# Kernel tuning notes

Hardware: AMD Instinct MI355X
Metric: run time of the kernel (lower is better)

The kernel has to match this reference:

```python
import jax, jax.numpy as jnp
import numpy as np

EPS = 1e-12  # F.normalize clamp eps
LOGIT_SCALE = float(np.exp(np.log(100.0)))  # coattn_logit_scale.exp() == 100.0


def _l2norm(x):
    n = jnp.linalg.norm(x, axis=-1, keepdims=True)
    return x / jnp.maximum(n, EPS)


def setup_inputs() -> dict:
    key = jax.random.key(0)
    k1, k2, k3, k4 = jax.random.split(key, 4)
    B, N, C = 1, 100000, 1024
    NUM_QUERY = 10  # +1 gated query
    X = jax.random.normal(k1, (B, N, C), dtype=jnp.float32)
    Q = jax.random.normal(k2, (NUM_QUERY + 1, C), dtype=jnp.float32)
    W = jax.random.normal(k3, (C, C), dtype=jnp.float32) * (1.0 / np.sqrt(C))
    b = jax.random.normal(k4, (C,), dtype=jnp.float32) * 0.01
    return {"X": X, "Q": Q, "W": W, "b": b}


def reference(X, Q, W, b):
    # X: [1, N, C] bag features; Q: [num_query+1, C]; W,b: visual_adapter Linear
    Qn = _l2norm(Q)[None]            # [1, q+1, C]
    Xn = _l2norm(X)                  # [1, N, C]
    A_ = jnp.einsum('bqc,bnc->bqn', Qn, Xn)   # cosine similarities [1, q+1, N]
    # gated-query subtraction: last query's scores subtracted from the rest
    A_ = A_[:, :-1, :] - A_[:, -1:, :]        # [1, q, N]
    A = jax.nn.softmax(LOGIT_SCALE * A_, axis=-1)
    out = jnp.einsum('bqn,bnc->bqc', A, X)    # [1, q, C]
    pooled = jnp.mean(out, axis=1)            # 'mean' query pooling -> [1, C]
    return pooled @ W.T + b                   # visual_adapter (nn.Linear)
```

## Files before the change

### kernel.cpp

```cpp
#include <hip/hip_runtime.h>
#include <float.h>
#include <math.h>

#define C    1024
#define NQ   10
#define LGS  16
#define K1B  2048
#define K1W  (K1B * 4)
#define G4   512

template <int CTRL, int ROWM>
__device__ __forceinline__ float dpp_add(float x) {
  int mv = __builtin_amdgcn_update_dpp(0, __float_as_int(x), CTRL, ROWM, 0xf, true);
  return x + __int_as_float(mv);
}
__device__ __forceinline__ float wave_sum64(float x) {
  x = dpp_add<0xB1,  0xf>(x);
  x = dpp_add<0x4E,  0xf>(x);
  x = dpp_add<0x141, 0xf>(x);
  x = dpp_add<0x140, 0xf>(x);
  x = dpp_add<0x142, 0xa>(x);
  x = dpp_add<0x143, 0xc>(x);
  return __int_as_float(__builtin_amdgcn_readlane(__float_as_int(x), 63));
}

__global__ __launch_bounds__(256) void k0_qdiff(const float* __restrict__ Q,
                                                float* __restrict__ qd) {
  __shared__ float red[256];
  __shared__ float inorm[NQ + 1];
  int t = threadIdx.x;
  for (int k = 0; k <= NQ; ++k) {
    float s = 0.f;
    for (int c = t; c < C; c += 256) { float v = Q[k * C + c]; s = fmaf(v, v, s); }
    red[t] = s; __syncthreads();
    for (int st = 128; st > 0; st >>= 1) {
      if (t < st) red[t] += red[t + st];
      __syncthreads();
    }
    if (t == 0) inorm[k] = 1.0f / fmaxf(sqrtf(red[0]), 1e-12f);
    __syncthreads();
  }
  for (int k = 0; k < NQ; ++k)
    for (int c = t; c < C; c += 256)
      qd[k * C + c] = Q[k * C + c] * inorm[k] - Q[NQ * C + c] * inorm[NQ];
}

__global__ __launch_bounds__(256) void k1_logits(const float* __restrict__ X,
                                                 const float* __restrict__ qd,
                                                 float* __restrict__ Lg,
                                                 float* __restrict__ bmax,
                                                 int N) {
  const int t  = threadIdx.x;
  const int l  = t & 63, wv = t >> 6;
  const int w  = blockIdx.x * 4 + wv;
  const int co = l << 2;

  float4 q4[NQ][4];
#pragma unroll
  for (int k = 0; k < NQ; ++k)
#pragma unroll
    for (int j = 0; j < 4; ++j)
      q4[k][j] = *(const float4*)(qd + k * C + j * 256 + co);

  float mx[NQ];
#pragma unroll
  for (int k = 0; k < NQ; ++k) mx[k] = -FLT_MAX;

  for (int r = w; r < N; r += K1W) {
    const float* xp = X + (size_t)r * C + co;
    float4 xv[4];
#pragma unroll
    for (int j = 0; j < 4; ++j) xv[j] = *(const float4*)(xp + j * 256);

    float ss = 0.f;
    float dot[NQ];
#pragma unroll
    for (int k = 0; k < NQ; ++k) dot[k] = 0.f;
#pragma unroll
    for (int j = 0; j < 4; ++j) {
      float4 v = xv[j];
      ss = fmaf(v.x, v.x, fmaf(v.y, v.y, fmaf(v.z, v.z, fmaf(v.w, v.w, ss))));
#pragma unroll
      for (int k = 0; k < NQ; ++k) {
        float4 q = q4[k][j];
        dot[k] = fmaf(v.x, q.x, fmaf(v.y, q.y, fmaf(v.z, q.z, fmaf(v.w, q.w, dot[k]))));
      }
    }

    float ssu = wave_sum64(ss);
    float rn  = 100.0f / fmaxf(sqrtf(ssu), 1e-12f);
    float lg[NQ];
#pragma unroll
    for (int k = 0; k < NQ; ++k) {
      lg[k] = wave_sum64(dot[k]) * rn;
      mx[k] = fmaxf(mx[k], lg[k]);
    }
    if (l == 0) {
      float* lp = Lg + (size_t)r * LGS;
      *(float4*)(lp)     = make_float4(lg[0], lg[1], lg[2], lg[3]);
      *(float4*)(lp + 4) = make_float4(lg[4], lg[5], lg[6], lg[7]);
      *(float2*)(lp + 8) = make_float2(lg[8], lg[9]);
    }
  }

  __shared__ float sm[4][16];
  if (l == 0) {
#pragma unroll
    for (int k = 0; k < NQ; ++k) sm[wv][k] = mx[k];
  }
  __syncthreads();
  if (t < NQ) {
    float m = fmaxf(fmaxf(sm[0][t], sm[1][t]), fmaxf(sm[2][t], sm[3][t]));
    bmax[blockIdx.x * 16 + t] = m;
  }
}

__global__ __launch_bounds__(256) void k2_gmax(const float* __restrict__ bmax,
                                               float* __restrict__ M, int NB) {
  __shared__ float red[256];
  int k = blockIdx.x, t = threadIdx.x;
  float mm = -FLT_MAX;
  for (int i = t; i < NB; i += 256) mm = fmaxf(mm, bmax[i * 16 + k]);
  red[t] = mm; __syncthreads();
  for (int st = 128; st > 0; st >>= 1) {
    if (t < st) red[t] = fmaxf(red[t], red[t + st]);
    __syncthreads();
  }
  if (t == 0) M[k] = red[0];
}

__global__ __launch_bounds__(256) void k4_partial(const float* __restrict__ X,
                                                  const float* __restrict__ Lg,
                                                  const float* __restrict__ M,
                                                  float* __restrict__ partial,
                                                  float* __restrict__ dsum,
                                                  int N, int rpb) {
  int g = blockIdx.x, t = threadIdx.x;
  int n0 = g * rpb;
  int n1 = min(n0 + rpb, N);
  float m[NQ];
#pragma unroll
  for (int k = 0; k < NQ; ++k) m[k] = M[k];
  float a[NQ][4];
#pragma unroll
  for (int k = 0; k < NQ; ++k) { a[k][0] = 0.f; a[k][1] = 0.f; a[k][2] = 0.f; a[k][3] = 0.f; }
  float ds[NQ];
#pragma unroll
  for (int k = 0; k < NQ; ++k) ds[k] = 0.f;

#pragma unroll 2
  for (int n = n0; n < n1; ++n) {
    float4 x4 = *(const float4*)&X[(size_t)n * C + (t << 2)];
    float w[NQ];
#pragma unroll
    for (int k = 0; k < NQ; ++k) w[k] = __expf(Lg[(size_t)n * LGS + k] - m[k]);
#pragma unroll
    for (int k = 0; k < NQ; ++k) {
      ds[k] += w[k];
      a[k][0] = fmaf(w[k], x4.x, a[k][0]);
      a[k][1] = fmaf(w[k], x4.y, a[k][1]);
      a[k][2] = fmaf(w[k], x4.z, a[k][2]);
      a[k][3] = fmaf(w[k], x4.w, a[k][3]);
    }
  }
#pragma unroll
  for (int k = 0; k < NQ; ++k) {
    float4 o; o.x = a[k][0]; o.y = a[k][1]; o.z = a[k][2]; o.w = a[k][3];
    *(float4*)&partial[(((size_t)(g * NQ + k)) << 10) + (t << 2)] = o;
  }
  if (t == 0) {
#pragma unroll
    for (int k = 0; k < NQ; ++k) dsum[g * NQ + k] = ds[k];
  }
}

__global__ __launch_bounds__(256) void k5a_pooled(const float* __restrict__ partial,
                                                  const float* __restrict__ dsum,
                                                  float* __restrict__ pooled) {
  __shared__ float invD[NQ];
  __shared__ float r4[256][4];
  int t = threadIdx.x;
  if (t < NQ) {
    float s = 0.f;
    for (int g = 0; g < G4; ++g) s += dsum[g * NQ + t];
    invD[t] = 1.0f / (s * (float)NQ);
  }
  __syncthreads();
  int c0 = blockIdx.x * 4;
  float a0 = 0.f, a1 = 0.f, a2 = 0.f, a3 = 0.f;
  for (int idx = t; idx < G4 * NQ; idx += 256) {
    int k = idx % NQ;
    const float4 p = *(const float4*)&partial[(((size_t)idx) << 10) + c0];
    float s = invD[k];
    a0 = fmaf(p.x, s, a0); a1 = fmaf(p.y, s, a1);
    a2 = fmaf(p.z, s, a2); a3 = fmaf(p.w, s, a3);
  }
  r4[t][0] = a0; r4[t][1] = a1; r4[t][2] = a2; r4[t][3] = a3;
  __syncthreads();
  for (int st = 128; st > 0; st >>= 1) {
    if (t < st) {
      r4[t][0] += r4[t + st][0]; r4[t][1] += r4[t + st][1];
      r4[t][2] += r4[t + st][2]; r4[t][3] += r4[t + st][3];
    }
    __syncthreads();
  }
  if (t < 4) pooled[c0 + t] = r4[0][t];
}

__global__ __launch_bounds__(256) void k5b_out(const float* __restrict__ W,
                                               const float* __restrict__ bias,
                                               const float* __restrict__ pooled,
                                               float* __restrict__ out) {
  __shared__ float sp[C];
  int t = threadIdx.x;
  for (int i = t; i < C; i += 256) sp[i] = pooled[i];
  __syncthreads();
  int wv = t >> 6, lane = t & 63;
#pragma unroll
  for (int jj = 0; jj < 8; ++jj) {
    int j = blockIdx.x * 32 + wv * 8 + jj;
    float s = 0.f;
#pragma unroll
    for (int seg = 0; seg < 4; ++seg) {
      int cbase = seg * 256 + lane * 4;
      float4 w4 = *(const float4*)&W[(size_t)j * C + cbase];
      float4 p4 = *(const float4*)&sp[cbase];
      s += w4.x * p4.x + w4.y * p4.y + w4.z * p4.z + w4.w * p4.w;
    }
#pragma unroll
    for (int off = 32; off > 0; off >>= 1) s += __shfl_down(s, off);
    if (lane == 0) out[j] = s + bias[j];
  }
}

extern "C" void kernel_launch(void* const* d_in, const int* in_sizes, int n_in,
                              void* d_out, int out_size, void* d_ws, size_t ws_size,
                              hipStream_t stream) {
  const float* X = (const float*)d_in[0];
  const float* Q = (const float*)d_in[1];
  const float* W = (const float*)d_in[2];
  const float* b = (const float*)d_in[3];
  float* out = (float*)d_out;

  int N = in_sizes[0] / C;
  int rpb = (N + G4 - 1) / G4;

  float* ws      = (float*)d_ws;
  float* qd      = ws;
  float* M       = qd + NQ * C;
  float* bmax    = M + 16;
  float* dsum    = bmax + K1B * 16;
  float* pooled  = dsum + G4 * NQ;
  float* Lg      = pooled + C;
  float* partial = Lg + (size_t)N * LGS;

  hipLaunchKernelGGL(k0_qdiff,  dim3(1),      dim3(256), 0, stream, Q, qd);
  hipLaunchKernelGGL(k1_logits, dim3(K1B),    dim3(256), 0, stream, X, qd, Lg, bmax, N);
  hipLaunchKernelGGL(k2_gmax,   dim3(NQ),     dim3(256), 0, stream, bmax, M, K1B);
  hipLaunchKernelGGL(k4_partial,dim3(G4),     dim3(256), 0, stream, X, Lg, M, partial, dsum, N, rpb);
  hipLaunchKernelGGL(k5a_pooled,dim3(C / 4),  dim3(256), 0, stream, partial, dsum, pooled);
  hipLaunchKernelGGL(k5b_out,   dim3(C / 32), dim3(256), 0, stream, W, b, pooled, out);
}
```

Before: 747.7 us.

## Fuse logit and weighted-sum passes with online softmax per block

Merges the logit kernel, the global-max kernel and the partial-accumulation kernel into one kernel that runs online softmax. Each block handles a contiguous row range in chunks of 25 rows: it computes logits into LDS, rescales its accumulators whenever the running max changes, then accumulates exp-weighted X while the chunk is still hot in cache. The pooling kernel then merges per-block maxima and rescales the partial sums. This removes the second full HBM read of X (about 400MB) and the logits buffer round-trip. The cost is extra block-wide syncs per chunk and only 500 blocks, each with heavy register pressure.

```diff
diff --git a/kernel.cpp b/kernel.cpp
--- a/kernel.cpp
+++ b/kernel.cpp
@@ -4,10 +4,9 @@
 
 #define C    1024
 #define NQ   10
+#define G4   500
 #define LGS  16
-#define K1B  2048
-#define K1W  (K1B * 4)
-#define G4   512
+#define RSUB 25
 
 template <int CTRL, int ROWM>
 __device__ __forceinline__ float dpp_add(float x) {
@@ -45,124 +44,120 @@
       qd[k * C + c] = Q[k * C + c] * inorm[k] - Q[NQ * C + c] * inorm[NQ];
 }
 
-__global__ __launch_bounds__(256) void k1_logits(const float* __restrict__ X,
-                                                 const float* __restrict__ qd,
-                                                 float* __restrict__ Lg,
-                                                 float* __restrict__ bmax,
-                                                 int N) {
-  const int t  = threadIdx.x;
-  const int l  = t & 63, wv = t >> 6;
-  const int w  = blockIdx.x * 4 + wv;
+__global__ __launch_bounds__(256, 2) void kf_fused(const float* __restrict__ X,
+                                                   const float* __restrict__ qd,
+                                                   float* __restrict__ partial,
+                                                   float* __restrict__ dsum,
+                                                   float* __restrict__ mblk,
+                                                   int N, int rpb) {
+  __shared__ float lgbuf[2][RSUB][LGS];
+  __shared__ float wmS[4][8];
+  __shared__ float sMnew[16];
+
+  const int g = blockIdx.x, t = threadIdx.x;
+  const int l = t & 63, wv = t >> 6;
+  const int pr = wv >> 1;
+  const int qbase = (wv & 1) * 5;
   const int co = l << 2;
 
-  float4 q4[NQ][4];
-#pragma unroll
-  for (int k = 0; k < NQ; ++k)
+  const int n0 = g * rpb;
+  const int n1 = min(n0 + rpb, N);
+
+  float4 q4[5][4];
+#pragma unroll
+  for (int k = 0; k < 5; ++k)
 #pragma unroll
     for (int j = 0; j < 4; ++j)
-      q4[k][j] = *(const float4*)(qd + k * C + j * 256 + co);
-
-  float mx[NQ];
-#pragma unroll
-  for (int k = 0; k < NQ; ++k) mx[k] = -FLT_MAX;
-
-  for (int r = w; r < N; r += K1W) {
-    const float* xp = X + (size_t)r * C + co;
-    float4 xv[4];
-#pragma unroll
-    for (int j = 0; j < 4; ++j) xv[j] = *(const float4*)(xp + j * 256);
-
-    float ss = 0.f;
-    float dot[NQ];
-#pragma unroll
-    for (int k = 0; k < NQ; ++k) dot[k] = 0.f;
-#pragma unroll
-    for (int j = 0; j < 4; ++j) {
-      float4 v = xv[j];
-      ss = fmaf(v.x, v.x, fmaf(v.y, v.y, fmaf(v.z, v.z, fmaf(v.w, v.w, ss))));
-#pragma unroll
-      for (int k = 0; k < NQ; ++k) {
-        float4 q = q4[k][j];
-        dot[k] = fmaf(v.x, q.x, fmaf(v.y, q.y, fmaf(v.z, q.z, fmaf(v.w, q.w, dot[k]))));
+      q4[k][j] = *(const float4*)(qd + (qbase + k) * C + j * 256 + co);
+
+  float a[NQ][4], ds[NQ], mo[NQ];
+#pragma unroll
+  for (int k = 0; k < NQ; ++k) {
+    a[k][0] = a[k][1] = a[k][2] = a[k][3] = 0.f;
+    ds[k] = 0.f; mo[k] = -FLT_MAX;
+  }
+
+  int s = 0;
+  for (int c0 = n0; c0 < n1; c0 += RSUB) {
+    const int cnt = min(RSUB, n1 - c0);
+
+    float wmx[5];
+#pragma unroll
+    for (int k = 0; k < 5; ++k) wmx[k] = -FLT_MAX;
+
+    for (int i = pr; i < cnt; i += 2) {
+      const float* xp = X + (size_t)(c0 + i) * C + co;
+      float4 xv[4];
+#pragma unroll
+      for (int j = 0; j < 4; ++j) xv[j] = *(const float4*)(xp + j * 256);
+
+      float ss = 0.f, dot[5];
+#pragma unroll
+      for (int k = 0; k < 5; ++k) dot[k] = 0.f;
+#pragma unroll
+      for (int j = 0; j < 4; ++j) {
+        float4 v = xv[j];
+        ss = fmaf(v.x, v.x, fmaf(v.y, v.y, fmaf(v.z, v.z, fmaf(v.w, v.w, ss))));
+#pragma unroll
+        for (int k = 0; k < 5; ++k) {
+          float4 q = q4[k][j];
+          dot[k] = fmaf(v.x, q.x, fmaf(v.y, q.y, fmaf(v.z, q.z, fmaf(v.w, q.w, dot[k]))));
+        }
       }
-    }
-
-    float ssu = wave_sum64(ss);
-    float rn  = 100.0f / fmaxf(sqrtf(ssu), 1e-12f);
-    float lg[NQ];
+      float ssu = wave_sum64(ss);
+      float rn  = 100.0f / fmaxf(sqrtf(ssu), 1e-12f);
+#pragma unroll
+      for (int k = 0; k < 5; ++k) {
+        float lg = wave_sum64(dot[k]) * rn;
+        wmx[k] = fmaxf(wmx[k], lg);
+        if (l == 0) lgbuf[s][i][qbase + k] = lg;
+      }
+    }
+    if (l == 0) {
+#pragma unroll
+      for (int k = 0; k < 5; ++k) wmS[wv][k] = wmx[k];
+    }
+    __syncthreads();
+
 #pragma unroll
     for (int k = 0; k < NQ; ++k) {
-      lg[k] = wave_sum64(dot[k]) * rn;
-      mx[k] = fmaxf(mx[k], lg[k]);
-    }
-    if (l == 0) {
-      float* lp = Lg + (size_t)r * LGS;
-      *(float4*)(lp)     = make_float4(lg[0], lg[1], lg[2], lg[3]);
-      *(float4*)(lp + 4) = make_float4(lg[4], lg[5], lg[6], lg[7]);
-      *(float2*)(lp + 8) = make_float2(lg[8], lg[9]);
-    }
-  }
-
-  __shared__ float sm[4][16];
-  if (l == 0) {
-#pragma unroll
-    for (int k = 0; k < NQ; ++k) sm[wv][k] = mx[k];
-  }
-  __syncthreads();
-  if (t < NQ) {
-    float m = fmaxf(fmaxf(sm[0][t], sm[1][t]), fmaxf(sm[2][t], sm[3][t]));
-    bmax[blockIdx.x * 16 + t] = m;
-  }
-}
-
-__global__ __launch_bounds__(256) void k2_gmax(const float* __restrict__ bmax,
-                                               float* __restrict__ M, int NB) {
-  __shared__ float red[256];
-  int k = blockIdx.x, t = threadIdx.x;
-  float mm = -FLT_MAX;
-  for (int i = t; i < NB; i += 256) mm = fmaxf(mm, bmax[i * 16 + k]);
-  red[t] = mm; __syncthreads();
-  for (int st = 128; st > 0; st >>= 1) {
-    if (t < st) red[t] = fmaxf(red[t], red[t + st]);
-    __syncthreads();
-  }
-  if (t == 0) M[k] = red[0];
-}
-
-__global__ __launch_bounds__(256) void k4_partial(const float* __restrict__ X,
-                                                  const float* __restrict__ Lg,
-                                                  const float* __restrict__ M,
-                                                  float* __restrict__ partial,
-                                                  float* __restrict__ dsum,
-                                                  int N, int rpb) {
-  int g = blockIdx.x, t = threadIdx.x;
-  int n0 = g * rpb;
-  int n1 = min(n0 + rpb, N);
-  float m[NQ];
-#pragma unroll
-  for (int k = 0; k < NQ; ++k) m[k] = M[k];
-  float a[NQ][4];
-#pragma unroll
-  for (int k = 0; k < NQ; ++k) { a[k][0] = 0.f; a[k][1] = 0.f; a[k][2] = 0.f; a[k][3] = 0.f; }
-  float ds[NQ];
-#pragma unroll
-  for (int k = 0; k < NQ; ++k) ds[k] = 0.f;
+      float cm = (k < 5) ? fmaxf(wmS[0][k], wmS[2][k])
+                         : fmaxf(wmS[1][k - 5], wmS[3][k - 5]);
+      float mn = fmaxf(mo[k], cm);
+      float sc = __expf(mo[k] - mn);
+      ds[k] *= sc;
+      a[k][0] *= sc; a[k][1] *= sc; a[k][2] *= sc; a[k][3] *= sc;
+      mo[k] = mn;
+      if (t == 0) sMnew[k] = mn;
+    }
+    __syncthreads();
+
+    for (int idx = t; idx < cnt * LGS; idx += 256) {
+      int rr = idx >> 4, k = idx & 15;
+      if (k < NQ) lgbuf[s][rr][k] = __expf(lgbuf[s][rr][k] - sMnew[k]);
+    }
+    __syncthreads();
 
 #pragma unroll 2
-  for (int n = n0; n < n1; ++n) {
-    float4 x4 = *(const float4*)&X[(size_t)n * C + (t << 2)];
-    float w[NQ];
-#pragma unroll
-    for (int k = 0; k < NQ; ++k) w[k] = __expf(Lg[(size_t)n * LGS + k] - m[k]);
-#pragma unroll
-    for (int k = 0; k < NQ; ++k) {
-      ds[k] += w[k];
-      a[k][0] = fmaf(w[k], x4.x, a[k][0]);
-      a[k][1] = fmaf(w[k], x4.y, a[k][1]);
-      a[k][2] = fmaf(w[k], x4.z, a[k][2]);
-      a[k][3] = fmaf(w[k], x4.w, a[k][3]);
-    }
-  }
+    for (int i = 0; i < cnt; ++i) {
+      float4 x4 = *(const float4*)&X[(size_t)(c0 + i) * C + (t << 2)];
+      float4 wA = *(const float4*)&lgbuf[s][i][0];
+      float4 wB = *(const float4*)&lgbuf[s][i][4];
+      float2 wC = *(const float2*)&lgbuf[s][i][8];
+#define ACC(K, W)                                            \
+      ds[K] += (W);                                          \
+      a[K][0] = fmaf((W), x4.x, a[K][0]);                    \
+      a[K][1] = fmaf((W), x4.y, a[K][1]);                    \
+      a[K][2] = fmaf((W), x4.z, a[K][2]);                    \
+      a[K][3] = fmaf((W), x4.w, a[K][3]);
+      ACC(0, wA.x) ACC(1, wA.y) ACC(2, wA.z) ACC(3, wA.w)
+      ACC(4, wB.x) ACC(5, wB.y) ACC(6, wB.z) ACC(7, wB.w)
+      ACC(8, wC.x) ACC(9, wC.y)
+#undef ACC
+    }
+    s ^= 1;
+  }
+
 #pragma unroll
   for (int k = 0; k < NQ; ++k) {
     float4 o; o.x = a[k][0]; o.y = a[k][1]; o.z = a[k][2]; o.w = a[k][3];
@@ -170,30 +165,56 @@
   }
   if (t == 0) {
 #pragma unroll
-    for (int k = 0; k < NQ; ++k) dsum[g * NQ + k] = ds[k];
+    for (int k = 0; k < NQ; ++k) {
+      dsum[g * NQ + k] = ds[k];
+      mblk[g * 16 + k] = mo[k];
+    }
   }
 }
 
 __global__ __launch_bounds__(256) void k5a_pooled(const float* __restrict__ partial,
                                                   const float* __restrict__ dsum,
+                                                  const float* __restrict__ mblk,
                                                   float* __restrict__ pooled) {
-  __shared__ float invD[NQ];
+  __shared__ float sM[16], sF[16];
+  __shared__ float red[256];
   __shared__ float r4[256][4];
   int t = threadIdx.x;
-  if (t < NQ) {
-    float s = 0.f;
-    for (int g = 0; g < G4; ++g) s += dsum[g * NQ + t];
-    invD[t] = 1.0f / (s * (float)NQ);
-  }
-  __syncthreads();
+  int k = t & 15, grp = t >> 4;
+
+  float mm = -FLT_MAX;
+  if (k < NQ)
+    for (int g = grp; g < G4; g += 16) mm = fmaxf(mm, mblk[g * 16 + k]);
+  red[t] = mm; __syncthreads();
+  if (t < 16) {
+    float m2 = red[t];
+    for (int j = 1; j < 16; ++j) m2 = fmaxf(m2, red[t + 16 * j]);
+    sM[t] = m2;
+  }
+  __syncthreads();
+
+  float dd = 0.f;
+  if (k < NQ) {
+    float Mk = sM[k];
+    for (int g = grp; g < G4; g += 16)
+      dd += dsum[g * NQ + k] * __expf(mblk[g * 16 + k] - Mk);
+  }
+  red[t] = dd; __syncthreads();
+  if (t < 16) {
+    float d2 = 0.f;
+    for (int j = 0; j < 16; ++j) d2 += red[t + 16 * j];
+    sF[t] = 1.0f / ((float)NQ * d2);
+  }
+  __syncthreads();
+
   int c0 = blockIdx.x * 4;
   float a0 = 0.f, a1 = 0.f, a2 = 0.f, a3 = 0.f;
   for (int idx = t; idx < G4 * NQ; idx += 256) {
-    int k = idx % NQ;
+    int g = idx / NQ, kq = idx - g * NQ;
+    float f = __expf(mblk[g * 16 + kq] - sM[kq]) * sF[kq];
     const float4 p = *(const float4*)&partial[(((size_t)idx) << 10) + c0];
-    float s = invD[k];
-    a0 = fmaf(p.x, s, a0); a1 = fmaf(p.y, s, a1);
-    a2 = fmaf(p.z, s, a2); a3 = fmaf(p.w, s, a3);
+    a0 = fmaf(p.x, f, a0); a1 = fmaf(p.y, f, a1);
+    a2 = fmaf(p.z, f, a2); a3 = fmaf(p.w, f, a3);
   }
   r4[t][0] = a0; r4[t][1] = a1; r4[t][2] = a2; r4[t][3] = a3;
   __syncthreads();
@@ -242,22 +263,20 @@
   const float* b = (const float*)d_in[3];
   float* out = (float*)d_out;
 
-  int N = in_sizes[0] / C;
+  int N   = in_sizes[0] / C;
   int rpb = (N + G4 - 1) / G4;
 
   float* ws      = (float*)d_ws;
   float* qd      = ws;
-  float* M       = qd + NQ * C;
-  float* bmax    = M + 16;
-  float* dsum    = bmax + K1B * 16;
+  float* mblk    = qd + NQ * C;
+  float* dsum    = mblk + G4 * 16;
   float* pooled  = dsum + G4 * NQ;
-  float* Lg      = pooled + C;
-  float* partial = Lg + (size_t)N * LGS;
+  float* partial = pooled + C;
 
   hipLaunchKernelGGL(k0_qdiff,  dim3(1),      dim3(256), 0, stream, Q, qd);
-  hipLaunchKernelGGL(k1_logits, dim3(K1B),    dim3(256), 0, stream, X, qd, Lg, bmax, N);
-  hipLaunchKernelGGL(k2_gmax,   dim3(NQ),     dim3(256), 0, stream, bmax, M, K1B);
-  hipLaunchKernelGGL(k4_partial,dim3(G4),     dim3(256), 0, stream, X, Lg, M, partial, dsum, N, rpb);
-  hipLaunchKernelGGL(k5a_pooled,dim3(C / 4),  dim3(256), 0, stream, partial, dsum, pooled);
+  hipLaunchKernelGGL(kf_fused,  dim3(G4),     dim3(256), 0, stream,
+                     X, qd, partial, dsum, mblk, N, rpb);
+  hipLaunchKernelGGL(k5a_pooled,dim3(C / 4),  dim3(256), 0, stream,
+                     partial, dsum, mblk, pooled);
   hipLaunchKernelGGL(k5b_out,   dim3(C / 32), dim3(256), 0, stream, W, b, pooled, out);
 }
```

After: 696.8 us. -6.8%, faster.
